# Performance work log

Hardware: AMD Instinct MI355X
Metric: run time of the kernel (lower is better)

The kernel has to match this reference:

```python
import jax, jax.numpy as jnp
import numpy as np

B, S, D = 4, 2048, 1152
H, KVH, HD = 16, 4, 64
SW = 1792
NEG = jnp.float32(-1e9)


def setup_inputs() -> dict:
    key = jax.random.key(0)
    ks = jax.random.split(key, 6)
    x = jax.random.normal(ks[0], (B, S, D), jnp.float32)
    s = 0.02
    wq = jax.random.normal(ks[1], (H * HD, D), jnp.float32) * s
    wk = jax.random.normal(ks[2], (KVH * HD, D), jnp.float32) * s
    wv = jax.random.normal(ks[3], (KVH * HD, D), jnp.float32) * s
    wo = jax.random.normal(ks[4], (D, H * HD), jnp.float32) * s
    # rotary freqs: theta=10000, standard llama-style
    inv = 1.0 / (10000.0 ** (np.arange(0, HD, 2, dtype=np.float32) / HD))
    t = np.arange(S, dtype=np.float32)
    fr = np.outer(t, inv)  # [S, HD//2]
    freqs_cos = jnp.asarray(np.cos(fr), jnp.float32)
    freqs_sin = jnp.asarray(np.sin(fr), jnp.float32)
    positions = jnp.arange(S, dtype=jnp.int32)
    # sliding-window causal additive mask: attend j iff 0 <= i-j < SW
    i = jnp.arange(S)[:, None]
    j = jnp.arange(S)[None, :]
    allowed = (j <= i) & (i - j < SW)
    mask = jnp.where(allowed, jnp.float32(0.0), NEG)
    cache_k = jnp.zeros((B, SW, KVH, HD), jnp.float32)
    cache_v = jnp.zeros((B, SW, KVH, HD), jnp.float32)
    return {"x": x, "wq": wq, "wk": wk, "wv": wv, "wo": wo,
            "freqs_cos": freqs_cos, "freqs_sin": freqs_sin, "mask": mask,
            "cache_k": cache_k, "cache_v": cache_v, "positions": positions}


def _rope(t, cos, sin):
    # t: [B,S,h,HD]; complex multiply on (even, odd) pairs
    tr = t.reshape(t.shape[:-1] + (HD // 2, 2))
    a, b = tr[..., 0], tr[..., 1]
    c = cos[None, :, None, :]
    s = sin[None, :, None, :]
    out = jnp.stack([a * c - b * s, a * s + b * c], axis=-1)
    return out.reshape(t.shape)


def reference(x, wq, wk, wv, wo, freqs_cos, freqs_sin, mask, cache_k, cache_v, positions):
    bsz, seqlen, _ = x.shape
    xq = jnp.einsum('bsd,ed->bse', x, wq).reshape(bsz, seqlen, H, HD)
    xk = jnp.einsum('bsd,ed->bse', x, wk).reshape(bsz, seqlen, KVH, HD)
    xv = jnp.einsum('bsd,ed->bse', x, wv).reshape(bsz, seqlen, KVH, HD)
    xq = _rope(xq, freqs_cos, freqs_sin)
    xk = _rope(xk, freqs_cos, freqs_sin)
    # circular-buffer cache scatter (last SW tokens, modulo indexing)
    idx = positions[-SW:] % SW
    new_ck = cache_k.at[:, idx].set(xk[:, -SW:])
    new_cv = cache_v.at[:, idx].set(xv[:, -SW:])
    # GQA: expand kv heads (repeat_interleave on head dim)
    rep = H // KVH
    key = jnp.repeat(xk, rep, axis=2)   # [B,S,H,HD]
    value = jnp.repeat(xv, rep, axis=2)
    q = xq.transpose(0, 2, 1, 3)        # [B,H,S,HD]
    k = key.transpose(0, 2, 1, 3)
    v = value.transpose(0, 2, 1, 3)
    scale = 1.0 / jnp.sqrt(jnp.float32(HD))
    scores = jnp.einsum('bhqd,bhkd->bhqk', q, k) * scale + mask[None, None]
    probs = jax.nn.softmax(scores, axis=-1)
    out = jnp.einsum('bhqk,bhkd->bhqd', probs, v)
    out = out.transpose(0, 2, 1, 3).reshape(bsz, seqlen, H * HD)
    out = jnp.einsum('bse,de->bsd', out, wo)
    return out, new_ck, new_cv
```

## Files before the change

kernel.cpp:

```cpp
#include <hip/hip_runtime.h>
#include <cstdint>
#include <cstddef>


typedef unsigned short u16;
typedef unsigned int   u32;
typedef __attribute__((ext_vector_type(8))) short bf16x8;
typedef __attribute__((ext_vector_type(4))) float f32x4;

#define AS1(p) ((const __attribute__((address_space(1))) void*)(p))
#define AS3(p) ((__attribute__((address_space(3))) void*)(p))

__device__ __forceinline__ u16 f2bf(float f) {
  u32 u = __float_as_uint(f);
  u += 0x7fffu + ((u >> 16) & 1u);
  return (u16)(u >> 16);
}
__device__ __forceinline__ float bf2f(u32 x) { return __uint_as_float(x << 16); }
__device__ __forceinline__ f32x4 mfma16(bf16x8 a, bf16x8 b, f32x4 c) {
  return __builtin_amdgcn_mfma_f32_16x16x32_bf16(a, b, c, 0, 0, 0);
}
__device__ __forceinline__ u32 cvtpk_bf16(float lo, float hi) {
  u32 r;
  asm("v_cvt_pk_bf16_f32 %0, %1, %2" : "=v"(r) : "v"(lo), "v"(hi));
  return r;
}

__global__ __launch_bounds__(256) void cvt5_kernel(const float* __restrict__ x,
                                                   const float* __restrict__ wq,
                                                   const float* __restrict__ wk,
                                                   const float* __restrict__ wv,
                                                   const float* __restrict__ wo,
                                                   u16* __restrict__ xb,
                                                   u16* __restrict__ wqkvb,
                                                   u16* __restrict__ wob) {
  int i = blockIdx.x * 256 + threadIdx.x;
  const float* in; u16* out; int off;
  if (i < 2359296)      { in = x;  out = xb;                  off = i; }
  else if (i < 2654208) { in = wq; out = wqkvb;               off = i - 2359296; }
  else if (i < 2727936) { in = wk; out = wqkvb + 1024 * 1152; off = i - 2654208; }
  else if (i < 2801664) { in = wv; out = wqkvb + 1280 * 1152; off = i - 2727936; }
  else                  { in = wo; out = wob;                 off = i - 2801664; }
  float4 v = ((const float4*)in)[off];
  uint2 o;
  o.x = (u32)f2bf(v.x) | ((u32)f2bf(v.y) << 16);
  o.y = (u32)f2bf(v.z) | ((u32)f2bf(v.w) << 16);
  ((uint2*)out)[off] = o;
}

template<int BF16_OUT>
__global__ __launch_bounds__(256) void gemm_bt(const u16* __restrict__ A,
                                               const u16* __restrict__ B,
                                               void* __restrict__ C,
                                               int M, int N, int K, int NT) {
  __shared__ u16 As[128][64];
  __shared__ u16 Bs[128][64];
  const int tid  = threadIdx.x;
  const int w    = tid >> 6, lane = tid & 63;
  const int l15  = lane & 15, hi4 = lane >> 4;
  const int lid  = blockIdx.x;
  const int k_   = lid >> 3;
  const int by   = (lid & 7) + 8 * (k_ / NT);
  const int bx   = k_ % NT;
  const int m0   = by * 128, n0 = bx * 128;
  const int wr   = w >> 1, wc = w & 1;

  const int srow = lane >> 3;
  const int scol = ((lane & 7) ^ srow) << 3;
  const u16* Ab = A + (size_t)(m0 + w * 32 + srow) * K + scol;
  const u16* Bb = B + (size_t)(n0 + w * 32 + srow) * K + scol;
  u16* AsDst = &As[w * 32][0];
  u16* BsDst = &Bs[w * 32][0];

  const int swz = (l15 & 7) << 4;
  const int c0  = (((hi4 * 16)      ^ swz) >> 1);
  const int c1  = (((64 + hi4 * 16) ^ swz) >> 1);
  const u16* aRd = &As[wr * 64 + l15][0];
  const u16* bRd = &Bs[wc * 64 + l15][0];

  f32x4 acc[4][4] = {};

  for (int kk = 0; kk < K; kk += 64) {
#pragma unroll
    for (int q = 0; q < 4; q++) {
      __builtin_amdgcn_global_load_lds(AS1(Ab + kk + (size_t)q * 8 * K),
                                       AS3(AsDst + q * 8 * 64), 16, 0, 0);
      __builtin_amdgcn_global_load_lds(AS1(Bb + kk + (size_t)q * 8 * K),
                                       AS3(BsDst + q * 8 * 64), 16, 0, 0);
    }
    __syncthreads();
#pragma unroll
    for (int ks = 0; ks < 2; ks++) {
      const int cc = ks ? c1 : c0;
      bf16x8 af[4], bfr[4];
#pragma unroll
      for (int t = 0; t < 4; t++) af[t]  = *(const bf16x8*)(aRd + t * 16 * 64 + cc);
#pragma unroll
      for (int t = 0; t < 4; t++) bfr[t] = *(const bf16x8*)(bRd + t * 16 * 64 + cc);
#pragma unroll
      for (int mi = 0; mi < 4; mi++)
#pragma unroll
        for (int ni = 0; ni < 4; ni++)
          acc[mi][ni] = mfma16(af[mi], bfr[ni], acc[mi][ni]);
    }
    __syncthreads();
  }

#pragma unroll
  for (int mi = 0; mi < 4; mi++) {
#pragma unroll
    for (int r = 0; r < 4; r++) {
      int row = m0 + wr * 64 + mi * 16 + hi4 * 4 + r;
      size_t base = (size_t)row * N + n0 + wc * 64 + l15;
#pragma unroll
      for (int ni = 0; ni < 4; ni++) {
        float v = acc[mi][ni][r];
        if (BF16_OUT) ((u16*)C)[base + ni * 16] = f2bf(v);
        else          ((float*)C)[base + ni * 16] = v;
      }
    }
  }
}

__global__ __launch_bounds__(256) void ropev_kernel(u16* __restrict__ buf,
                                                    float* __restrict__ kcache,
                                                    u16* __restrict__ vT,
                                                    float* __restrict__ ncv,
                                                    const float* __restrict__ cosT,
                                                    const float* __restrict__ sinT) {
  __shared__ u16 tile[64][65];
  if (blockIdx.x < 20480) {
    int idx = blockIdx.x * 256 + threadIdx.x;
    const bool isQ = idx < 4194304;
    int pi = isQ ? idx : idx - 4194304;
    int m  = isQ ? (pi >> 9) : (pi >> 7);
    int p  = isQ ? (pi & 511) : (pi & 127);
    int coloff = isQ ? 0 : 512;
    int s = m & 2047, b = m >> 11;
    int hh = p & 31;
    u32* bp = (u32*)buf + (size_t)m * 768 + coloff + p;
    u32 pk = *bp;
    float a  = bf2f(pk & 0xffffu), bb = bf2f(pk >> 16);
    float c  = cosT[s * 32 + hh],  sn = sinT[s * 32 + hh];
    float o0 = a * c - bb * sn;
    float o1 = a * sn + bb * c;
    const float qs = isQ ? 0.18033688011112042f : 1.0f;
    *bp = (u32)f2bf(o0 * qs) | ((u32)f2bf(o1 * qs) << 16);
    if (!isQ && s >= 256) {
      int pc = (s < 1792) ? s : s - 1792;
      float2* cp = (float2*)(kcache + (size_t)(b * 1792 + pc) * 256 + 2 * p);
      *cp = make_float2(o0, o1);
    }
  } else {
    int bi = blockIdx.x - 20480;
    int s0 = (bi & 31) * 64, kvh = (bi >> 5) & 3, b = bi >> 7;
    int t = threadIdx.x;
    int r = t >> 2, cc = (t & 3) * 16;
    const u16* src = buf + (size_t)(b * 2048 + s0 + r) * 1536 + 1280 + kvh * 64 + cc;
    uint4 v0 = *(const uint4*)src;
    uint4 v1 = *(const uint4*)(src + 8);
    u16 vals[16];
    *(uint4*)&vals[0] = v0;
    *(uint4*)&vals[8] = v1;
    int s = s0 + r;
    if (s >= 256) {
      int pc = (s < 1792) ? s : s - 1792;
      float* dst = ncv + (size_t)(b * 1792 + pc) * 256 + kvh * 64 + cc;
#pragma unroll
      for (int i = 0; i < 16; i += 4) {
        float4 f = make_float4(bf2f(vals[i]), bf2f(vals[i + 1]),
                               bf2f(vals[i + 2]), bf2f(vals[i + 3]));
        *(float4*)(dst + i) = f;
      }
    }
#pragma unroll
    for (int i = 0; i < 16; i++) tile[cc + i][r] = vals[i];
    __syncthreads();
    u16 ov[16];
#pragma unroll
    for (int i = 0; i < 16; i++) {
      int p = cc + i;
      int pg = p & 31, e = pg & 7, g = pg >> 3;
      int key = (p & ~31) + ((e < 4) ? (4 * g + e) : (16 + 4 * g + (e - 4)));
      ov[i] = tile[r][key];
    }
    u16* dst2 = vT + (size_t)((b * 4 + kvh) * 64 + r) * 2048 + s0 + cc;
    *(uint4*)dst2 = *(uint4*)&ov[0];
    *(uint4*)(dst2 + 8) = *(uint4*)&ov[8];
  }
}

__global__ __launch_bounds__(256) void attn_kernel(const u16* __restrict__ qkv,
                                                   const u16* __restrict__ vT,
                                                   u16* __restrict__ attnb) {
  __shared__ __align__(16) u16 Kbuf[2][64][64];
  __shared__ __align__(16) u16 Vbuf[2][64][64];
  const int tid = threadIdx.x;
  const int w = tid >> 6, lane = tid & 63;
  const int l15 = lane & 15, hi4 = lane >> 4;

  const int lid  = blockIdx.x;
  const int wgid = (lid & 7) * 128 + (lid >> 3);
  const int gx   = wgid & 63;
  const int rr   = wgid >> 6;
  const int kvh  = rr & 3, b = rr >> 2;
  const int i0   = 32 * (63 - gx);
  const int h    = kvh * 4 + w;

  const u16* qbase = qkv + (size_t)(b * 2048) * 1536 + h * 64;
  const u16* kbase = qkv + (size_t)(b * 2048) * 1536 + 1024 + kvh * 64;
  const u16* vbase = vT + (size_t)((b * 4 + kvh) * 64) * 2048;

  bf16x8 qa[2][2];
  {
    const u16* qp = qbase + (size_t)(i0 + l15) * 1536 + hi4 * 8;
#pragma unroll
    for (int m = 0; m < 2; m++)
#pragma unroll
      for (int ki = 0; ki < 2; ki++)
        qa[m][ki] = *(const bf16x8*)(qp + m * 16 * 1536 + ki * 32);
  }

  bf16x8 ones;
#pragma unroll
  for (int i = 0; i < 8; i++) ones[i] = (short)0x3F80;

  f32x4 o[2][4] = {};
  f32x4 ol[2] = {};

  const int srow = lane >> 3;
  const int ssl  = (lane & 7) ^ srow;

#define STAGE(J0, BS)                                                                     \
  do {                                                                                    \
    _Pragma("unroll")                                                                     \
    for (int q = 0; q < 2; q++) {                                                         \
      const int row = 32 * q + 8 * w + srow;                                              \
      __builtin_amdgcn_global_load_lds(AS1(kbase + (size_t)((J0) + row) * 1536 + ssl * 8),\
                                       AS3(&Kbuf[BS][32 * q + 8 * w][0]), 16, 0, 0);      \
      __builtin_amdgcn_global_load_lds(AS1(vbase + (size_t)row * 2048 + (J0) + ssl * 8),  \
                                       AS3(&Vbuf[BS][32 * q + 8 * w][0]), 16, 0, 0);      \
    }                                                                                     \
  } while (0)

  int jstart = i0 - 1791;
  if (jstart < 0) jstart = 0;
  jstart &= ~63;
  const int jend = i0 + 32;
  const int ntiles = (jend - jstart + 63) >> 6;

  STAGE(jstart, 0);
  if (ntiles > 1) STAGE(jstart + 64, 1);

  for (int t = 0; t < ntiles; t++) {
    const int j0 = jstart + 64 * t;
    if (t + 1 < ntiles) asm volatile("s_waitcnt vmcnt(4)" ::: "memory");
    else                asm volatile("s_waitcnt vmcnt(0)" ::: "memory");
    __builtin_amdgcn_s_barrier();
    __builtin_amdgcn_sched_barrier(0);

    const u16* Kb = &Kbuf[t & 1][0][0];
    const u16* Vb = &Vbuf[t & 1][0][0];

    bf16x8 kf[2][4];
#pragma unroll
    for (int nt = 0; nt < 4; nt++)
#pragma unroll
      for (int ki = 0; ki < 2; ki++)
        kf[ki][nt] = *(const bf16x8*)(Kb + (nt * 16 + l15) * 64 +
                                      (((ki * 4 + hi4) ^ (l15 & 7)) << 3));

    bf16x8 vf[2][4];
#pragma unroll
    for (int tt = 0; tt < 4; tt++) {
      const int row = tt * 16 + l15;
#pragma unroll
      for (int kbp = 0; kbp < 2; kbp++)
        vf[kbp][tt] = *(const bf16x8*)(Vb + row * 64 +
                                       (((kbp * 4 + hi4) ^ (l15 & 7)) << 3));
    }

    __builtin_amdgcn_s_setprio(1);
    const bool fast = (j0 + 63 <= i0) && (i0 + 31 - j0 < 1792);
#pragma unroll
    for (int m = 0; m < 2; m++) {
      __align__(16) u32 pkb[8];
#pragma unroll
      for (int nt = 0; nt < 4; nt++) {
        f32x4 s = {0.f, 0.f, 0.f, 0.f};
        s = mfma16(kf[0][nt], qa[m][0], s);
        s = mfma16(kf[1][nt], qa[m][1], s);
        float p[4];
        if (fast) {
#pragma unroll
          for (int r = 0; r < 4; r++) p[r] = __builtin_amdgcn_exp2f(s[r]);
        } else {
          const int i = i0 + m * 16 + l15;
#pragma unroll
          for (int r = 0; r < 4; r++) {
            const int j = j0 + nt * 16 + hi4 * 4 + r;
            p[r] = (j <= i && i - j < 1792) ? __builtin_amdgcn_exp2f(s[r]) : 0.f;
          }
        }
        pkb[nt * 2]     = cvtpk_bf16(p[0], p[1]);
        pkb[nt * 2 + 1] = cvtpk_bf16(p[2], p[3]);
      }
      bf16x8 pa0 = *(const bf16x8*)&pkb[0];
      bf16x8 pa1 = *(const bf16x8*)&pkb[4];
#pragma unroll
      for (int tt = 0; tt < 4; tt++) {
        o[m][tt] = mfma16(pa0, vf[0][tt], o[m][tt]);
        o[m][tt] = mfma16(pa1, vf[1][tt], o[m][tt]);
      }
      ol[m] = mfma16(pa0, ones, ol[m]);
      ol[m] = mfma16(pa1, ones, ol[m]);
    }
    __builtin_amdgcn_s_setprio(0);

    __builtin_amdgcn_s_barrier();
    __builtin_amdgcn_sched_barrier(0);
    if (t + 2 < ntiles) STAGE(j0 + 128, t & 1);
  }
#undef STAGE

  u16* op = attnb + (size_t)(b * 2048 + i0 + hi4 * 4) * 1024 + h * 64 + l15;
#pragma unroll
  for (int m = 0; m < 2; m++)
#pragma unroll
    for (int r = 0; r < 4; r++) {
      float inv = 1.0f / ol[m][r];
#pragma unroll
      for (int tt = 0; tt < 4; tt++)
        op[(size_t)(m * 16 + r) * 1024 + 16 * tt] = f2bf(o[m][tt][r] * inv);
    }
}

extern "C" void kernel_launch(void* const* d_in, const int* in_sizes, int n_in,
                              void* d_out, int out_size, void* d_ws, size_t ws_size,
                              hipStream_t stream) {
  const float* x  = (const float*)d_in[0];
  const float* wq = (const float*)d_in[1];
  const float* wk = (const float*)d_in[2];
  const float* wv = (const float*)d_in[3];
  const float* wo = (const float*)d_in[4];
  const float* fc = (const float*)d_in[5];
  const float* fs = (const float*)d_in[6];

  float* out = (float*)d_out;
  float* nck = out + 9437184;
  float* ncv = nck + 1835008;

  char* ws = (char*)d_ws;
  u16* attnb = (u16*)(ws);
  u16* xb    = (u16*)(ws);
  u16* wqkvb = (u16*)(ws + 18874368);
  u16* wob   = (u16*)(ws + 22413312);
  u16* qkv   = (u16*)(ws + 24772608);
  u16* vT    = (u16*)(ws + 49938432);

  cvt5_kernel<<<12096, 256, 0, stream>>>(x, wq, wk, wv, wo, xb, wqkvb, wob);

  gemm_bt<1><<<768, 256, 0, stream>>>(xb, wqkvb, qkv, 8192, 1536, 1152, 12);

  ropev_kernel<<<20992, 256, 0, stream>>>(qkv, nck, vT, ncv, fc, fs);

  attn_kernel<<<1024, 256, 0, stream>>>(qkv, vT, attnb);

  gemm_bt<0><<<576, 256, 0, stream>>>(attnb, wob, out, 8192, 1152, 1024, 9);
}
```

Measured before the change: 158.1 us.

## Process two query heads per wave in attention, halving block size

The attention kernel now launches 128 threads (2 waves) per block, and each wave handles two query heads of the same KV group instead of one. The K/V fragments loaded from LDS are reused across both heads, which halves LDS reads per unit of work, and each wave issues twice as many staging loads. In exchange, registers per wave roughly double (two sets of O accumulators and Q fragments), which may lower occupancy or cause spills, and each block has fewer waves to hide latency.

Result: slower. 189.5 us (+19.9%).

```diff
diff --git a/kernel.cpp b/kernel.cpp
--- a/kernel.cpp
+++ b/kernel.cpp
@@ -190,7 +190,7 @@
   }
 }
 
-__global__ __launch_bounds__(256) void attn_kernel(const u16* __restrict__ qkv,
+__global__ __launch_bounds__(128) void attn_kernel(const u16* __restrict__ qkv,
                                                    const u16* __restrict__ vT,
                                                    u16* __restrict__ attnb) {
   __shared__ __align__(16) u16 Kbuf[2][64][64];
@@ -205,28 +205,30 @@
   const int rr   = wgid >> 6;
   const int kvh  = rr & 3, b = rr >> 2;
   const int i0   = 32 * (63 - gx);
-  const int h    = kvh * 4 + w;
-
-  const u16* qbase = qkv + (size_t)(b * 2048) * 1536 + h * 64;
+  const int h0   = kvh * 4 + 2 * w;
+
+  const u16* qbase = qkv + (size_t)(b * 2048) * 1536 + h0 * 64;
   const u16* kbase = qkv + (size_t)(b * 2048) * 1536 + 1024 + kvh * 64;
   const u16* vbase = vT + (size_t)((b * 4 + kvh) * 64) * 2048;
 
-  bf16x8 qa[2][2];
+  bf16x8 qa[2][2][2];
   {
     const u16* qp = qbase + (size_t)(i0 + l15) * 1536 + hi4 * 8;
 #pragma unroll
-    for (int m = 0; m < 2; m++)
-#pragma unroll
-      for (int ki = 0; ki < 2; ki++)
-        qa[m][ki] = *(const bf16x8*)(qp + m * 16 * 1536 + ki * 32);
+    for (int hh = 0; hh < 2; hh++)
+#pragma unroll
+      for (int m = 0; m < 2; m++)
+#pragma unroll
+        for (int ki = 0; ki < 2; ki++)
+          qa[hh][m][ki] = *(const bf16x8*)(qp + hh * 64 + m * 16 * 1536 + ki * 32);
   }
 
   bf16x8 ones;
 #pragma unroll
   for (int i = 0; i < 8; i++) ones[i] = (short)0x3F80;
 
-  f32x4 o[2][4] = {};
-  f32x4 ol[2] = {};
+  f32x4 o[2][2][4] = {};
+  f32x4 ol[2][2] = {};
 
   const int srow = lane >> 3;
   const int ssl  = (lane & 7) ^ srow;
@@ -234,12 +236,12 @@
 #define STAGE(J0, BS)                                                                     \
   do {                                                                                    \
     _Pragma("unroll")                                                                     \
-    for (int q = 0; q < 2; q++) {                                                         \
-      const int row = 32 * q + 8 * w + srow;                                              \
+    for (int q = 0; q < 4; q++) {                                                         \
+      const int row = 32 * w + 8 * q + srow;                                              \
       __builtin_amdgcn_global_load_lds(AS1(kbase + (size_t)((J0) + row) * 1536 + ssl * 8),\
-                                       AS3(&Kbuf[BS][32 * q + 8 * w][0]), 16, 0, 0);      \
+                                       AS3(&Kbuf[BS][32 * w + 8 * q][0]), 16, 0, 0);      \
       __builtin_amdgcn_global_load_lds(AS1(vbase + (size_t)row * 2048 + (J0) + ssl * 8),  \
-                                       AS3(&Vbuf[BS][32 * q + 8 * w][0]), 16, 0, 0);      \
+                                       AS3(&Vbuf[BS][32 * w + 8 * q][0]), 16, 0, 0);      \
     }                                                                                     \
   } while (0)
 
@@ -254,7 +256,7 @@
 
   for (int t = 0; t < ntiles; t++) {
     const int j0 = jstart + 64 * t;
-    if (t + 1 < ntiles) asm volatile("s_waitcnt vmcnt(4)" ::: "memory");
+    if (t + 1 < ntiles) asm volatile("s_waitcnt vmcnt(8)" ::: "memory");
     else                asm volatile("s_waitcnt vmcnt(0)" ::: "memory");
     __builtin_amdgcn_s_barrier();
     __builtin_amdgcn_sched_barrier(0);
@@ -283,37 +285,40 @@
     __builtin_amdgcn_s_setprio(1);
     const bool fast = (j0 + 63 <= i0) && (i0 + 31 - j0 < 1792);
 #pragma unroll
-    for (int m = 0; m < 2; m++) {
-      __align__(16) u32 pkb[8];
-#pragma unroll
-      for (int nt = 0; nt < 4; nt++) {
-        f32x4 s = {0.f, 0.f, 0.f, 0.f};
-        s = mfma16(kf[0][nt], qa[m][0], s);
-        s = mfma16(kf[1][nt], qa[m][1], s);
-        float p[4];
-        if (fast) {
-#pragma unroll
-          for (int r = 0; r < 4; r++) p[r] = __builtin_amdgcn_exp2f(s[r]);
-        } else {
-          const int i = i0 + m * 16 + l15;
-#pragma unroll
-          for (int r = 0; r < 4; r++) {
-            const int j = j0 + nt * 16 + hi4 * 4 + r;
-            p[r] = (j <= i && i - j < 1792) ? __builtin_amdgcn_exp2f(s[r]) : 0.f;
+    for (int hh = 0; hh < 2; hh++) {
+#pragma unroll
+      for (int m = 0; m < 2; m++) {
+        __align__(16) u32 pkb[8];
+#pragma unroll
+        for (int nt = 0; nt < 4; nt++) {
+          f32x4 s = {0.f, 0.f, 0.f, 0.f};
+          s = mfma16(kf[0][nt], qa[hh][m][0], s);
+          s = mfma16(kf[1][nt], qa[hh][m][1], s);
+          float p[4];
+          if (fast) {
+#pragma unroll
+            for (int r = 0; r < 4; r++) p[r] = __builtin_amdgcn_exp2f(s[r]);
+          } else {
+            const int i = i0 + m * 16 + l15;
+#pragma unroll
+            for (int r = 0; r < 4; r++) {
+              const int j = j0 + nt * 16 + hi4 * 4 + r;
+              p[r] = (j <= i && i - j < 1792) ? __builtin_amdgcn_exp2f(s[r]) : 0.f;
+            }
           }
+          pkb[nt * 2]     = cvtpk_bf16(p[0], p[1]);
+          pkb[nt * 2 + 1] = cvtpk_bf16(p[2], p[3]);
         }
-        pkb[nt * 2]     = cvtpk_bf16(p[0], p[1]);
-        pkb[nt * 2 + 1] = cvtpk_bf16(p[2], p[3]);
+        bf16x8 pa0 = *(const bf16x8*)&pkb[0];
+        bf16x8 pa1 = *(const bf16x8*)&pkb[4];
+#pragma unroll
+        for (int tt = 0; tt < 4; tt++) {
+          o[hh][m][tt] = mfma16(pa0, vf[0][tt], o[hh][m][tt]);
+          o[hh][m][tt] = mfma16(pa1, vf[1][tt], o[hh][m][tt]);
+        }
+        ol[hh][m] = mfma16(pa0, ones, ol[hh][m]);
+        ol[hh][m] = mfma16(pa1, ones, ol[hh][m]);
       }
-      bf16x8 pa0 = *(const bf16x8*)&pkb[0];
-      bf16x8 pa1 = *(const bf16x8*)&pkb[4];
-#pragma unroll
-      for (int tt = 0; tt < 4; tt++) {
-        o[m][tt] = mfma16(pa0, vf[0][tt], o[m][tt]);
-        o[m][tt] = mfma16(pa1, vf[1][tt], o[m][tt]);
-      }
-      ol[m] = mfma16(pa0, ones, ol[m]);
-      ol[m] = mfma16(pa1, ones, ol[m]);
     }
     __builtin_amdgcn_s_setprio(0);
 
@@ -323,16 +328,19 @@
   }
 #undef STAGE
 
-  u16* op = attnb + (size_t)(b * 2048 + i0 + hi4 * 4) * 1024 + h * 64 + l15;
-#pragma unroll
-  for (int m = 0; m < 2; m++)
-#pragma unroll
-    for (int r = 0; r < 4; r++) {
-      float inv = 1.0f / ol[m][r];
-#pragma unroll
-      for (int tt = 0; tt < 4; tt++)
-        op[(size_t)(m * 16 + r) * 1024 + 16 * tt] = f2bf(o[m][tt][r] * inv);
-    }
+#pragma unroll
+  for (int hh = 0; hh < 2; hh++) {
+    u16* op = attnb + (size_t)(b * 2048 + i0 + hi4 * 4) * 1024 + (h0 + hh) * 64 + l15;
+#pragma unroll
+    for (int m = 0; m < 2; m++)
+#pragma unroll
+      for (int r = 0; r < 4; r++) {
+        float inv = 1.0f / ol[hh][m][r];
+#pragma unroll
+        for (int tt = 0; tt < 4; tt++)
+          op[(size_t)(m * 16 + r) * 1024 + 16 * tt] = f2bf(o[hh][m][tt][r] * inv);
+      }
+  }
 }
 
 extern "C" void kernel_launch(void* const* d_in, const int* in_sizes, int n_in,
@@ -364,7 +372,7 @@
 
   ropev_kernel<<<20992, 256, 0, stream>>>(qkv, nck, vT, ncv, fc, fs);
 
-  attn_kernel<<<1024, 256, 0, stream>>>(qkv, vT, attnb);
+  attn_kernel<<<1024, 128, 0, stream>>>(qkv, vT, attnb);
 
   gemm_bt<0><<<576, 256, 0, stream>>>(attnb, wob, out, 8192, 1152, 1024, 9);
 }
```
